# Kernel tuning notes

Measured on AMD Instinct MI355X. Metric: run time of the kernel, lower is better.

Reference implementation:

```python
import jax, jax.numpy as jnp
import numpy as np

EMB_DIM = 128
MID = 192  # ceil(1.5 * emb_dim)
VOCAB = 3000
KCLS = 5
B = 16
S = 128
EPS = 1e-5


def _linear_init(k, fin, fout):
    k1, k2 = jax.random.split(k)
    bound = 1.0 / np.sqrt(fin)
    W = jax.random.uniform(k1, (fin, fout), minval=-bound, maxval=bound, dtype=jnp.float32)
    b = jax.random.uniform(k2, (fout,), minval=-bound, maxval=bound, dtype=jnp.float32)
    return W, b


def setup_inputs() -> dict:
    key = jax.random.key(0)
    ks = jax.random.split(key, 7)
    emb = jax.random.normal(ks[0], (VOCAB, EMB_DIM), dtype=jnp.float32)
    W1, b1 = _linear_init(ks[1], 2 * EMB_DIM, MID)   # encoder layer 1
    W2, b2 = _linear_init(ks[2], MID, EMB_DIM)       # encoder layer 2
    W3, b3 = _linear_init(ks[3], EMB_DIM, MID)       # decoder layer 1
    W4, b4 = _linear_init(ks[4], MID, 2 * EMB_DIM)   # decoder layer 2
    Wk, bk = _linear_init(ks[5], EMB_DIM, KCLS)      # soft head
    inputs = jax.random.randint(ks[6], (B, S), 0, VOCAB, dtype=jnp.int64)
    return dict(inputs=inputs, emb=emb, W1=W1, b1=b1, W2=W2, b2=b2,
                W3=W3, b3=b3, W4=W4, b4=b4, Wk=Wk, bk=bk)


def _forward(inputs, emb, W1, b1, W2, b2, W3, b3, W4, b4, Wk, bk):
    X = emb[inputs]                      # (B,S,m)
    Bs, Sl, m = X.shape
    bidx = jnp.arange(Bs)
    karr = jnp.arange(Sl)
    jarr = jnp.arange(Sl - 1)

    def step(carry, t):
        nodes, counts, acc = carry       # (B,S,m), (B,S), (B,)
        L = Sl - t                       # current active list length
        right, left = nodes[:, 1:], nodes[:, :-1]          # pair j = (node[j+1], node[j])
        y = (jnp.concatenate([right, left], -1) @ W1 + b1) @ W2 + b2   # (B,S-1,m)
        xx = (y @ W3 + b3) @ W4 + b4                                    # (B,S-1,2m)
        # torch cross_entropy with float-vector target: -sum(target * log_softmax(input))
        ls1 = -(right * jax.nn.log_softmax(xx[..., :m], -1)).sum(-1)
        ls2 = -(left * jax.nn.log_softmax(xx[..., m:], -1)).sum(-1)
        n1, n2 = counts[:, 1:], counts[:, :-1]
        loss = ((n1 + EPS) * ls1 + (n2 + EPS) * ls2) / (n1 + n2 + EPS)
        valid = jarr < (L - 1)                                          # only first L-1 pairs active
        idx = jnp.argmin(jnp.where(valid[None, :], loss, jnp.inf), axis=1)  # (B,)
        acc = acc + jnp.take_along_axis(loss, idx[:, None], 1)[:, 0]
        father_x = jnp.take_along_axis(y, idx[:, None, None], 1)[:, 0]  # (B,m)
        # faithful bug: lc = nodelist[idx-1] (python wrap to L-1 when idx==0), rc = nodelist[idx]
        lc_idx = jnp.where(idx == 0, L - 1, idx - 1)
        father_cnt = (jnp.take_along_axis(counts, idx[:, None], 1)[:, 0]
                      + jnp.take_along_axis(counts, lc_idx[:, None], 1)[:, 0])
        pos = jnp.maximum(idx - 1, 0)
        # new list: drop lc and rc, father lands at pos; gather map reproduces list insert/remove
        src = jnp.where((idx[:, None] == 0) | (karr[None, :] < idx[:, None] - 1),
                        karr[None, :], karr[None, :] + 1)
        src = jnp.minimum(src, Sl - 1)
        nodes = jnp.take_along_axis(nodes, src[:, :, None], 1).at[bidx, pos].set(father_x)
        counts = jnp.take_along_axis(counts, src, 1).at[bidx, pos].set(father_cnt)
        return (nodes, counts, acc), None

    init = (X, jnp.ones((Bs, Sl), X.dtype), jnp.zeros((Bs,), X.dtype))
    (nodes, counts, acc), _ = jax.lax.scan(step, init, jnp.arange(Sl - 1))
    pred = jnp.argmax(nodes[:, 0] @ Wk + bk, axis=-1)   # argmax softmax == argmax logits
    return pred, acc.sum() / Bs


def reference(inputs, emb, W1, b1, W2, b2, W3, b3, W4, b4, Wk, bk):
    return _forward(inputs, emb, W1, b1, W2, b2, W3, b3, W4, b4, Wk, bk)
```

## Files before the change

kernel.cpp:

```cpp
#include <hip/hip_runtime.h>
#include <math.h>

#define EMB 128
#define MID 192
#define SEQ 128
#define BATCH 16
#define NPAIR 127
#define KCLS 5
#define EPSF 1e-5f

#define OFF_WYT   0
#define OFF_BY    32768
#define OFF_WXXT  32896
#define OFF_BXX   65664
#define OFF_NODES 65920
#define OFF_YC    328064
#define OFF_L0    588160

__global__ void k_comp(const float* __restrict__ W1, const float* __restrict__ b1,
                       const float* __restrict__ W2, const float* __restrict__ b2,
                       const float* __restrict__ W3, const float* __restrict__ b3,
                       const float* __restrict__ W4, const float* __restrict__ b4,
                       float* __restrict__ ws) {
    int tid = blockIdx.x * blockDim.x + threadIdx.x;
    if (tid < 32768) {
        int k = tid >> 7, o = tid & 127;
        float a = 0.f;
        for (int j = 0; j < MID; ++j) a += W1[k*MID+j] * W2[j*EMB+o];
        int q = k >> 6, jj = k & 63;
        ws[OFF_WYT + (size_t)(q*128 + o)*64 + jj] = a;
    } else if (tid < 65536) {
        int t = tid - 32768;
        int k = t >> 8, c = t & 255;
        float a = 0.f;
        for (int j = 0; j < MID; ++j) a += W3[k*MID+j] * W4[j*256+c];
        int hh = k >> 6, jj = k & 63;
        ws[OFF_WXXT + (size_t)(hh*256 + c)*64 + jj] = a;
    } else if (tid < 65536 + 128) {
        int o = tid - 65536;
        float a = b2[o];
        for (int j = 0; j < MID; ++j) a += b1[j] * W2[j*EMB+o];
        ws[OFF_BY + o] = a;
    } else if (tid < 65536 + 128 + 256) {
        int o = tid - 65536 - 128;
        float a = b4[o];
        for (int j = 0; j < MID; ++j) a += b3[j] * W4[j*256+o];
        ws[OFF_BXX + o] = a;
    }
}

__global__ void k_nodes(const int* __restrict__ inp, const float* __restrict__ emb,
                        float* __restrict__ ws) {
    int tid = blockIdx.x * blockDim.x + threadIdx.x;
    if (tid >= BATCH*SEQ*EMB) return;
    int d = tid & 127;
    int bs = tid >> 7;
    int tok = inp[bs];
    ws[OFF_NODES + tid] = emb[tok*EMB + d];
}

__global__ void __launch_bounds__(512, 2) k_init(float* __restrict__ ws) {
    __shared__ float s_x[2][2*EMB];
    __shared__ float s_red[4][2][EMB];
    __shared__ float s_redx[2][2][256];
    __shared__ float s_y[2][EMB];
    __shared__ float s_by[EMB];
    __shared__ float s_bxx[2*EMB];
    __shared__ float s_ls[2][2];
    int tid = threadIdx.x;
    int b = blockIdx.x >> 4, g = blockIdx.x & 15;
    float4 wy4[16], wxx4[16];
    {
        const float4* gw = (const float4*)(ws + OFF_WYT) + (size_t)tid*16;
        #pragma unroll
        for (int i = 0; i < 16; ++i) wy4[i] = gw[i];
        const float4* gx = (const float4*)(ws + OFF_WXXT) + (size_t)tid*16;
        #pragma unroll
        for (int i = 0; i < 16; ++i) wxx4[i] = gx[i];
    }
    if (tid < EMB) s_by[tid] = ws[OFF_BY + tid];
    if (tid < 2*EMB) s_bxx[tid] = ws[OFF_BXX + tid];
    const float* nodes = ws + OFF_NODES + (size_t)b*SEQ*EMB;
    float* yc = ws + OFF_YC + (size_t)b*NPAIR*EMB;
    int q4 = tid >> 7, o = tid & 127;
    int hh = tid >> 8, c = tid & 255;
    int p_s = tid >> 8, kk = tid & 255;
    __syncthreads();
    for (int it = 0; it < 4; ++it) {
        int base = g*8 + it*2;
        {
            int j = base + p_s;
            int jj = j < NPAIR ? j : NPAIR - 1;
            s_x[p_s][kk] = nodes[(jj + (kk < 128 ? 1 : 0))*EMB + (kk & 127)];
        }
        __syncthreads();
        {
            const float4* sx4 = (const float4*)s_x;
            float a0 = 0.f, a1 = 0.f;
            #pragma unroll
            for (int i = 0; i < 16; ++i) {
                float4 w = wy4[i];
                float4 x0 = sx4[q4*16 + i];
                float4 x1 = sx4[64 + q4*16 + i];
                a0 += x0.x*w.x + x0.y*w.y + x0.z*w.z + x0.w*w.w;
                a1 += x1.x*w.x + x1.y*w.y + x1.z*w.z + x1.w*w.w;
            }
            s_red[q4][0][o] = a0;
            s_red[q4][1][o] = a1;
        }
        __syncthreads();
        if (tid < 256) {
            int p = tid >> 7, oo = tid & 127;
            float yv = s_red[0][p][oo] + s_red[1][p][oo] + s_red[2][p][oo] + s_red[3][p][oo] + s_by[oo];
            s_y[p][oo] = yv;
            int j2 = base + p;
            if (j2 < NPAIR) yc[(size_t)j2*EMB + oo] = yv;
        }
        __syncthreads();
        {
            const float4* sy4 = (const float4*)s_y;
            float c0 = 0.f, c1 = 0.f;
            #pragma unroll
            for (int i = 0; i < 16; ++i) {
                float4 w = wxx4[i];
                float4 y0 = sy4[hh*16 + i];
                float4 y1 = sy4[32 + hh*16 + i];
                c0 += y0.x*w.x + y0.y*w.y + y0.z*w.z + y0.w*w.w;
                c1 += y1.x*w.x + y1.y*w.y + y1.z*w.z + y1.w*w.w;
            }
            s_redx[hh][0][c] = c0;
            s_redx[hh][1][c] = c1;
        }
        __syncthreads();
        if (tid < 256) {
            int w = tid >> 6, lane = tid & 63;
            int p2 = w >> 1, h2 = w & 1;
            int cA = h2*128 + lane, cB = cA + 64;
            float v0 = s_redx[0][p2][cA] + s_redx[1][p2][cA] + s_bxx[cA];
            float v1 = s_redx[0][p2][cB] + s_redx[1][p2][cB] + s_bxx[cB];
            float m = fmaxf(v0, v1);
            for (int s = 32; s; s >>= 1) m = fmaxf(m, __shfl_xor(m, s, 64));
            float se = expf(v0 - m) + expf(v1 - m);
            for (int s = 32; s; s >>= 1) se += __shfl_xor(se, s, 64);
            float lse = m + logf(se);
            float o0 = s_x[p2][cA], o1 = s_x[p2][cB];
            float term = o0*(v0 - lse) + o1*(v1 - lse);
            for (int s = 32; s; s >>= 1) term += __shfl_xor(term, s, 64);
            if (lane == 0) s_ls[p2][h2] = -term;
        }
        __syncthreads();
        if (tid < 2) {
            int j2 = base + tid;
            if (j2 < NPAIR) {
                float l = ((1.f+EPSF)*s_ls[tid][0] + (1.f+EPSF)*s_ls[tid][1]) / (2.f + EPSF);
                ws[OFF_L0 + b*NPAIR + j2] = l;
            }
        }
        __syncthreads();
    }
}

__global__ void __launch_bounds__(512, 2) k_seq(float* __restrict__ ws,
                      const float* __restrict__ Wk, const float* __restrict__ bkv,
                      float* __restrict__ out) {
    __shared__ float s_nodes[SEQ*EMB];
    __shared__ float s_yc[NPAIR*EMB];
    __shared__ float s_red[4][2][EMB];
    __shared__ float s_redx[2][2][256];
    __shared__ float s_y[2][EMB];
    __shared__ float s_by[EMB];
    __shared__ float s_bxx[2*EMB];
    __shared__ float s_ls[2][2];
    __shared__ float s_loss[NPAIR];
    __shared__ float s_cnt[SEQ];
    __shared__ int   s_nslot[SEQ];
    __shared__ int   s_yslot[NPAIR];
    __shared__ int   s_q[2];
    __shared__ float s_wv[2];
    __shared__ int   s_wi[2];
    __shared__ float s_log[KCLS];

    int tid = threadIdx.x;
    int b = blockIdx.x;
    float4 wy4[16], wxx4[16];
    {
        const float4* gw = (const float4*)(ws + OFF_WYT) + (size_t)tid*16;
        #pragma unroll
        for (int i = 0; i < 16; ++i) wy4[i] = gw[i];
        const float4* gx = (const float4*)(ws + OFF_WXXT) + (size_t)tid*16;
        #pragma unroll
        for (int i = 0; i < 16; ++i) wxx4[i] = gx[i];
    }
    {
        const float4* gn = (const float4*)(ws + OFF_NODES + (size_t)b*SEQ*EMB);
        float4* sn = (float4*)s_nodes;
        for (int i = tid; i < SEQ*EMB/4; i += 512) sn[i] = gn[i];
        const float4* gy = (const float4*)(ws + OFF_YC + (size_t)b*NPAIR*EMB);
        float4* sy = (float4*)s_yc;
        for (int i = tid; i < NPAIR*EMB/4; i += 512) sy[i] = gy[i];
    }
    if (tid < EMB) s_by[tid] = ws[OFF_BY + tid];
    if (tid < 2*EMB) s_bxx[tid] = ws[OFF_BXX + tid];
    if (tid < NPAIR) { s_loss[tid] = ws[OFF_L0 + b*NPAIR + tid]; s_yslot[tid] = tid; }
    if (tid < SEQ)   { s_cnt[tid] = 1.f; s_nslot[tid] = tid; }
    float acc = 0.f;
    int q4 = tid >> 7, o = tid & 127;
    int hh = tid >> 8, c = tid & 255;
    __syncthreads();

    #pragma unroll 1
    for (int t = 0; t < NPAIR; ++t) {
        int L = SEQ - t;
        if (t > 0) {
            {
                int r = (q4 < 2) ? 1 : 0;
                int half = q4 & 1;
                int slot0 = s_nslot[s_q[0] + r];
                int slot1 = s_nslot[s_q[1] + r];
                const float4* n4 = (const float4*)s_nodes;
                int base0 = slot0*32 + half*16;
                int base1 = slot1*32 + half*16;
                float a0 = 0.f, a1 = 0.f;
                #pragma unroll
                for (int i = 0; i < 16; ++i) {
                    float4 w = wy4[i];
                    float4 x0 = n4[base0 + i];
                    float4 x1 = n4[base1 + i];
                    a0 += x0.x*w.x + x0.y*w.y + x0.z*w.z + x0.w*w.w;
                    a1 += x1.x*w.x + x1.y*w.y + x1.z*w.z + x1.w*w.w;
                }
                s_red[q4][0][o] = a0;
                s_red[q4][1][o] = a1;
            }
            __syncthreads();
            if (tid < 256) {
                int p = tid >> 7, oo = tid & 127;
                float yv = s_red[0][p][oo] + s_red[1][p][oo] + s_red[2][p][oo] + s_red[3][p][oo] + s_by[oo];
                s_y[p][oo] = yv;
                s_yc[(size_t)s_yslot[s_q[p]]*EMB + oo] = yv;
            }
            __syncthreads();
            {
                const float4* sy4 = (const float4*)s_y;
                float c0 = 0.f, c1 = 0.f;
                #pragma unroll
                for (int i = 0; i < 16; ++i) {
                    float4 w = wxx4[i];
                    float4 y0 = sy4[hh*16 + i];
                    float4 y1 = sy4[32 + hh*16 + i];
                    c0 += y0.x*w.x + y0.y*w.y + y0.z*w.z + y0.w*w.w;
                    c1 += y1.x*w.x + y1.y*w.y + y1.z*w.z + y1.w*w.w;
                }
                s_redx[hh][0][c] = c0;
                s_redx[hh][1][c] = c1;
            }
            __syncthreads();
            if (tid < 256) {
                int w = tid >> 6, lane = tid & 63;
                int p2 = w >> 1, h2 = w & 1;
                int cA = h2*128 + lane, cB = cA + 64;
                float v0 = s_redx[0][p2][cA] + s_redx[1][p2][cA] + s_bxx[cA];
                float v1 = s_redx[0][p2][cB] + s_redx[1][p2][cB] + s_bxx[cB];
                float m = fmaxf(v0, v1);
                for (int s = 32; s; s >>= 1) m = fmaxf(m, __shfl_xor(m, s, 64));
                float se = expf(v0 - m) + expf(v1 - m);
                for (int s = 32; s; s >>= 1) se += __shfl_xor(se, s, 64);
                float lse = m + logf(se);
                int slot = s_nslot[s_q[p2] + (h2 == 0 ? 1 : 0)];
                float o0 = s_nodes[slot*EMB + lane];
                float o1 = s_nodes[slot*EMB + 64 + lane];
                float term = o0*(v0 - lse) + o1*(v1 - lse);
                for (int s = 32; s; s >>= 1) term += __shfl_xor(term, s, 64);
                if (lane == 0) s_ls[p2][h2] = -term;
            }
            __syncthreads();
        }
        if (tid < 128) {
            float v = INFINITY;
            if (tid < L-1) {
                v = s_loss[tid];
                if (t > 0 && (tid == s_q[0] || tid == s_q[1])) {
                    int which = (tid == s_q[0]) ? 0 : 1;
                    float n1 = s_cnt[tid+1], n2 = s_cnt[tid];
                    v = ((n1+EPSF)*s_ls[which][0] + (n2+EPSF)*s_ls[which][1]) / (n1+n2+EPSF);
                    s_loss[tid] = v;
                }
            }
            int ii = tid;
            for (int s = 32; s; s >>= 1) {
                float ov = __shfl_xor(v, s, 64);
                int   oi = __shfl_xor(ii, s, 64);
                if (ov < v || (ov == v && oi < ii)) { v = ov; ii = oi; }
            }
            if ((tid & 63) == 0) { s_wv[tid>>6] = v; s_wi[tid>>6] = ii; }
        }
        __syncthreads();
        float bv0 = s_wv[0], bv1 = s_wv[1];
        int idx = (bv1 < bv0) ? s_wi[1] : s_wi[0];
        if (tid == 0) acc += fminf(bv0, bv1);
        int pos = idx > 0 ? idx - 1 : 0;
        int slotF = s_nslot[pos];
        int ysI   = s_yslot[idx];
        float fcnt = s_cnt[idx] + s_cnt[idx == 0 ? L-1 : idx-1];
        bool doShift = (idx > 0);
        bool shL = doShift && tid >= pos+1 && tid <= L-3;
        bool shC = doShift && tid >= pos+1 && tid <= L-2;
        float nl = 0.f, nc = 0.f; int nn = 0, ny = 0;
        if (shL) { nl = s_loss[tid+1]; ny = s_yslot[tid+1]; }
        if (shC) { nc = s_cnt[tid+1];  nn = s_nslot[tid+1]; }
        float fx = (tid < EMB) ? s_yc[(size_t)ysI*EMB + tid] : 0.f;
        __syncthreads();
        if (tid < EMB) s_nodes[slotF*EMB + tid] = fx;
        if (shL) { s_loss[tid] = nl; s_yslot[tid] = ny; }
        if (shC) { s_cnt[tid]  = nc; s_nslot[tid] = nn; }
        if (tid == 0) {
            s_cnt[pos] = fcnt;
            s_q[0] = (pos >= 1) ? pos - 1 : pos;
            s_q[1] = pos;
        }
        __syncthreads();
    }
    if (tid < KCLS) {
        int slot0 = s_nslot[0];
        float a = bkv[tid];
        for (int k = 0; k < EMB; ++k) a += s_nodes[slot0*EMB + k] * Wk[k*KCLS + tid];
        s_log[tid] = a;
    }
    __syncthreads();
    if (tid == 0) {
        int best = 0;
        for (int cc = 1; cc < KCLS; ++cc) if (s_log[cc] > s_log[best]) best = cc;
        out[b] = (float)best;
        atomicAdd(&out[BATCH], acc * (1.f/16.f));
    }
}

extern "C" void kernel_launch(void* const* d_in, const int* in_sizes, int n_in,
                              void* d_out, int out_size, void* d_ws, size_t ws_size,
                              hipStream_t stream) {
    const int*   inp = (const int*)d_in[0];
    const float* emb = (const float*)d_in[1];
    const float* W1  = (const float*)d_in[2];
    const float* b1  = (const float*)d_in[3];
    const float* W2  = (const float*)d_in[4];
    const float* b2  = (const float*)d_in[5];
    const float* W3  = (const float*)d_in[6];
    const float* b3  = (const float*)d_in[7];
    const float* W4  = (const float*)d_in[8];
    const float* b4  = (const float*)d_in[9];
    const float* Wk  = (const float*)d_in[10];
    const float* bk  = (const float*)d_in[11];
    float* out = (float*)d_out;
    float* ws  = (float*)d_ws;

    hipMemsetAsync(d_out, 0, (size_t)out_size * sizeof(float), stream);

    k_comp<<<(65920 + 255) / 256, 256, 0, stream>>>(W1, b1, W2, b2, W3, b3, W4, b4, ws);
    k_nodes<<<(BATCH*SEQ*EMB + 255) / 256, 256, 0, stream>>>(inp, emb, ws);
    k_init<<<BATCH * 16, 512, 0, stream>>>(ws);
    k_seq<<<BATCH, 512, 0, stream>>>(ws, Wk, bk, out);
}
```

Before: 566.0 us.

## Move decoder weight to LDS and keep node/pair state in global memory

```diff
diff --git a/kernel.cpp b/kernel.cpp
--- a/kernel.cpp
+++ b/kernel.cpp
@@ -11,7 +11,7 @@
 
 #define OFF_WYT   0
 #define OFF_BY    32768
-#define OFF_WXXT  32896
+#define OFF_WXX   32896
 #define OFF_BXX   65664
 #define OFF_NODES 65920
 #define OFF_YC    328064
@@ -34,8 +34,7 @@
         int k = t >> 8, c = t & 255;
         float a = 0.f;
         for (int j = 0; j < MID; ++j) a += W3[k*MID+j] * W4[j*256+c];
-        int hh = k >> 6, jj = k & 63;
-        ws[OFF_WXXT + (size_t)(hh*256 + c)*64 + jj] = a;
+        ws[OFF_WXX + (size_t)k*256 + c] = a;
     } else if (tid < 65536 + 128) {
         int o = tid - 65536;
         float a = b2[o];
@@ -60,6 +59,7 @@
 }
 
 __global__ void __launch_bounds__(512, 2) k_init(float* __restrict__ ws) {
+    __shared__ float s_wxx[128*256];
     __shared__ float s_x[2][2*EMB];
     __shared__ float s_red[4][2][EMB];
     __shared__ float s_redx[2][2][256];
@@ -69,14 +69,14 @@
     __shared__ float s_ls[2][2];
     int tid = threadIdx.x;
     int b = blockIdx.x >> 4, g = blockIdx.x & 15;
-    float4 wy4[16], wxx4[16];
+    float4 wy4[16];
     {
         const float4* gw = (const float4*)(ws + OFF_WYT) + (size_t)tid*16;
         #pragma unroll
         for (int i = 0; i < 16; ++i) wy4[i] = gw[i];
-        const float4* gx = (const float4*)(ws + OFF_WXXT) + (size_t)tid*16;
-        #pragma unroll
-        for (int i = 0; i < 16; ++i) wxx4[i] = gx[i];
+        const float4* gx = (const float4*)(ws + OFF_WXX);
+        float4* sw = (float4*)s_wxx;
+        for (int i = tid; i < 8192; i += 512) sw[i] = gx[i];
     }
     if (tid < EMB) s_by[tid] = ws[OFF_BY + tid];
     if (tid < 2*EMB) s_bxx[tid] = ws[OFF_BXX + tid];
@@ -118,15 +118,15 @@
         }
         __syncthreads();
         {
-            const float4* sy4 = (const float4*)s_y;
+            const float* wp = s_wxx + (hh << 6)*256 + c;
+            const float* yp0 = &s_y[0][hh << 6];
+            const float* yp1 = &s_y[1][hh << 6];
             float c0 = 0.f, c1 = 0.f;
             #pragma unroll
-            for (int i = 0; i < 16; ++i) {
-                float4 w = wxx4[i];
-                float4 y0 = sy4[hh*16 + i];
-                float4 y1 = sy4[32 + hh*16 + i];
-                c0 += y0.x*w.x + y0.y*w.y + y0.z*w.z + y0.w*w.w;
-                c1 += y1.x*w.x + y1.y*w.y + y1.z*w.z + y1.w*w.w;
+            for (int j = 0; j < 64; ++j) {
+                float w = wp[j*256];
+                c0 += yp0[j] * w;
+                c1 += yp1[j] * w;
             }
             s_redx[hh][0][c] = c0;
             s_redx[hh][1][c] = c1;
@@ -163,8 +163,8 @@
 __global__ void __launch_bounds__(512, 2) k_seq(float* __restrict__ ws,
                       const float* __restrict__ Wk, const float* __restrict__ bkv,
                       float* __restrict__ out) {
-    __shared__ float s_nodes[SEQ*EMB];
-    __shared__ float s_yc[NPAIR*EMB];
+    __shared__ float s_wxx[128*256];
+    __shared__ float s_x[2][2*EMB];
     __shared__ float s_red[4][2][EMB];
     __shared__ float s_redx[2][2][256];
     __shared__ float s_y[2][EMB];
@@ -182,23 +182,17 @@
 
     int tid = threadIdx.x;
     int b = blockIdx.x;
-    float4 wy4[16], wxx4[16];
+    float4 wy4[16];
     {
         const float4* gw = (const float4*)(ws + OFF_WYT) + (size_t)tid*16;
         #pragma unroll
         for (int i = 0; i < 16; ++i) wy4[i] = gw[i];
-        const float4* gx = (const float4*)(ws + OFF_WXXT) + (size_t)tid*16;
-        #pragma unroll
-        for (int i = 0; i < 16; ++i) wxx4[i] = gx[i];
-    }
-    {
-        const float4* gn = (const float4*)(ws + OFF_NODES + (size_t)b*SEQ*EMB);
-        float4* sn = (float4*)s_nodes;
-        for (int i = tid; i < SEQ*EMB/4; i += 512) sn[i] = gn[i];
-        const float4* gy = (const float4*)(ws + OFF_YC + (size_t)b*NPAIR*EMB);
-        float4* sy = (float4*)s_yc;
-        for (int i = tid; i < NPAIR*EMB/4; i += 512) sy[i] = gy[i];
-    }
+        const float4* gx = (const float4*)(ws + OFF_WXX);
+        float4* sw = (float4*)s_wxx;
+        for (int i = tid; i < 8192; i += 512) sw[i] = gx[i];
+    }
+    float* nodes = ws + OFF_NODES + (size_t)b*SEQ*EMB;
+    float* yc    = ws + OFF_YC    + (size_t)b*NPAIR*EMB;
     if (tid < EMB) s_by[tid] = ws[OFF_BY + tid];
     if (tid < 2*EMB) s_bxx[tid] = ws[OFF_BXX + tid];
     if (tid < NPAIR) { s_loss[tid] = ws[OFF_L0 + b*NPAIR + tid]; s_yslot[tid] = tid; }
@@ -206,6 +200,7 @@
     float acc = 0.f;
     int q4 = tid >> 7, o = tid & 127;
     int hh = tid >> 8, c = tid & 255;
+    int p_s = tid >> 8, kk = tid & 255;
     __syncthreads();
 
     #pragma unroll 1
@@ -213,19 +208,18 @@
         int L = SEQ - t;
         if (t > 0) {
             {
-                int r = (q4 < 2) ? 1 : 0;
-                int half = q4 & 1;
-                int slot0 = s_nslot[s_q[0] + r];
-                int slot1 = s_nslot[s_q[1] + r];
-                const float4* n4 = (const float4*)s_nodes;
-                int base0 = slot0*32 + half*16;
-                int base1 = slot1*32 + half*16;
+                int q = s_q[p_s];
+                s_x[p_s][kk] = nodes[s_nslot[q + (kk < 128 ? 1 : 0)]*EMB + (kk & 127)];
+            }
+            __syncthreads();
+            {
+                const float4* sx4 = (const float4*)s_x;
                 float a0 = 0.f, a1 = 0.f;
                 #pragma unroll
                 for (int i = 0; i < 16; ++i) {
                     float4 w = wy4[i];
-                    float4 x0 = n4[base0 + i];
-                    float4 x1 = n4[base1 + i];
+                    float4 x0 = sx4[q4*16 + i];
+                    float4 x1 = sx4[64 + q4*16 + i];
                     a0 += x0.x*w.x + x0.y*w.y + x0.z*w.z + x0.w*w.w;
                     a1 += x1.x*w.x + x1.y*w.y + x1.z*w.z + x1.w*w.w;
                 }
@@ -237,19 +231,19 @@
                 int p = tid >> 7, oo = tid & 127;
                 float yv = s_red[0][p][oo] + s_red[1][p][oo] + s_red[2][p][oo] + s_red[3][p][oo] + s_by[oo];
                 s_y[p][oo] = yv;
-                s_yc[(size_t)s_yslot[s_q[p]]*EMB + oo] = yv;
+                yc[(size_t)s_yslot[s_q[p]]*EMB + oo] = yv;
             }
             __syncthreads();
             {
-                const float4* sy4 = (const float4*)s_y;
+                const float* wp = s_wxx + (hh << 6)*256 + c;
+                const float* yp0 = &s_y[0][hh << 6];
+                const float* yp1 = &s_y[1][hh << 6];
                 float c0 = 0.f, c1 = 0.f;
                 #pragma unroll
-                for (int i = 0; i < 16; ++i) {
-                    float4 w = wxx4[i];
-                    float4 y0 = sy4[hh*16 + i];
-                    float4 y1 = sy4[32 + hh*16 + i];
-                    c0 += y0.x*w.x + y0.y*w.y + y0.z*w.z + y0.w*w.w;
-                    c1 += y1.x*w.x + y1.y*w.y + y1.z*w.z + y1.w*w.w;
+                for (int j = 0; j < 64; ++j) {
+                    float w = wp[j*256];
+                    c0 += yp0[j] * w;
+                    c1 += yp1[j] * w;
                 }
                 s_redx[hh][0][c] = c0;
                 s_redx[hh][1][c] = c1;
@@ -266,9 +260,7 @@
                 float se = expf(v0 - m) + expf(v1 - m);
                 for (int s = 32; s; s >>= 1) se += __shfl_xor(se, s, 64);
                 float lse = m + logf(se);
-                int slot = s_nslot[s_q[p2] + (h2 == 0 ? 1 : 0)];
-                float o0 = s_nodes[slot*EMB + lane];
-                float o1 = s_nodes[slot*EMB + 64 + lane];
+                float o0 = s_x[p2][cA], o1 = s_x[p2][cB];
                 float term = o0*(v0 - lse) + o1*(v1 - lse);
                 for (int s = 32; s; s >>= 1) term += __shfl_xor(term, s, 64);
                 if (lane == 0) s_ls[p2][h2] = -term;
@@ -308,9 +300,9 @@
         float nl = 0.f, nc = 0.f; int nn = 0, ny = 0;
         if (shL) { nl = s_loss[tid+1]; ny = s_yslot[tid+1]; }
         if (shC) { nc = s_cnt[tid+1];  nn = s_nslot[tid+1]; }
-        float fx = (tid < EMB) ? s_yc[(size_t)ysI*EMB + tid] : 0.f;
-        __syncthreads();
-        if (tid < EMB) s_nodes[slotF*EMB + tid] = fx;
+        float fx = (tid < EMB) ? yc[(size_t)ysI*EMB + tid] : 0.f;
+        __syncthreads();
+        if (tid < EMB) nodes[slotF*EMB + tid] = fx;
         if (shL) { s_loss[tid] = nl; s_yslot[tid] = ny; }
         if (shC) { s_cnt[tid]  = nc; s_nslot[tid] = nn; }
         if (tid == 0) {
@@ -323,7 +315,7 @@
     if (tid < KCLS) {
         int slot0 = s_nslot[0];
         float a = bkv[tid];
-        for (int k = 0; k < EMB; ++k) a += s_nodes[slot0*EMB + k] * Wk[k*KCLS + tid];
+        for (int k = 0; k < EMB; ++k) a += nodes[slot0*EMB + k] * Wk[k*KCLS + tid];
         s_log[tid] = a;
     }
     __syncthreads();
```

Result: slower. 636.2 us (+12.4%).

## Use 1024-thread blocks and double-buffer list state to drop a barrier

Applied to the files above, without the earlier changes.

```diff
diff --git a/kernel.cpp b/kernel.cpp
--- a/kernel.cpp
+++ b/kernel.cpp
@@ -11,7 +11,7 @@
 
 #define OFF_WYT   0
 #define OFF_BY    32768
-#define OFF_WXXT  32896
+#define OFF_WXX   32896
 #define OFF_BXX   65664
 #define OFF_NODES 65920
 #define OFF_YC    328064
@@ -27,15 +27,15 @@
         int k = tid >> 7, o = tid & 127;
         float a = 0.f;
         for (int j = 0; j < MID; ++j) a += W1[k*MID+j] * W2[j*EMB+o];
-        int q = k >> 6, jj = k & 63;
-        ws[OFF_WYT + (size_t)(q*128 + o)*64 + jj] = a;
+        int q8 = k >> 5, jj = k & 31;
+        ws[OFF_WYT + ((q8*128 + o) << 5) + jj] = a;
     } else if (tid < 65536) {
         int t = tid - 32768;
         int k = t >> 8, c = t & 255;
         float a = 0.f;
         for (int j = 0; j < MID; ++j) a += W3[k*MID+j] * W4[j*256+c];
-        int hh = k >> 6, jj = k & 63;
-        ws[OFF_WXXT + (size_t)(hh*256 + c)*64 + jj] = a;
+        int h4 = k >> 5, jj = k & 31;
+        ws[OFF_WXX + ((h4*256 + c) << 5) + jj] = a;
     } else if (tid < 65536 + 128) {
         int o = tid - 65536;
         float a = b2[o];
@@ -59,36 +59,36 @@
     ws[OFF_NODES + tid] = emb[tok*EMB + d];
 }
 
-__global__ void __launch_bounds__(512, 2) k_init(float* __restrict__ ws) {
+__global__ void __launch_bounds__(1024) k_init(float* __restrict__ ws) {
     __shared__ float s_x[2][2*EMB];
-    __shared__ float s_red[4][2][EMB];
-    __shared__ float s_redx[2][2][256];
+    __shared__ float s_red[8][2][EMB];
+    __shared__ float s_redx[4][2][256];
     __shared__ float s_y[2][EMB];
     __shared__ float s_by[EMB];
     __shared__ float s_bxx[2*EMB];
     __shared__ float s_ls[2][2];
     int tid = threadIdx.x;
     int b = blockIdx.x >> 4, g = blockIdx.x & 15;
-    float4 wy4[16], wxx4[16];
+    float4 wy8[8], wxx8[8];
     {
-        const float4* gw = (const float4*)(ws + OFF_WYT) + (size_t)tid*16;
+        const float4* gw = (const float4*)(ws + OFF_WYT) + (size_t)tid*8;
         #pragma unroll
-        for (int i = 0; i < 16; ++i) wy4[i] = gw[i];
-        const float4* gx = (const float4*)(ws + OFF_WXXT) + (size_t)tid*16;
+        for (int i = 0; i < 8; ++i) wy8[i] = gw[i];
+        const float4* gx = (const float4*)(ws + OFF_WXX) + (size_t)tid*8;
         #pragma unroll
-        for (int i = 0; i < 16; ++i) wxx4[i] = gx[i];
+        for (int i = 0; i < 8; ++i) wxx8[i] = gx[i];
     }
     if (tid < EMB) s_by[tid] = ws[OFF_BY + tid];
     if (tid < 2*EMB) s_bxx[tid] = ws[OFF_BXX + tid];
     const float* nodes = ws + OFF_NODES + (size_t)b*SEQ*EMB;
     float* yc = ws + OFF_YC + (size_t)b*NPAIR*EMB;
-    int q4 = tid >> 7, o = tid & 127;
-    int hh = tid >> 8, c = tid & 255;
-    int p_s = tid >> 8, kk = tid & 255;
+    int q8 = tid >> 7, o = tid & 127;
+    int h4 = tid >> 8, c = tid & 255;
     __syncthreads();
     for (int it = 0; it < 4; ++it) {
         int base = g*8 + it*2;
-        {
+        if (tid < 512) {
+            int p_s = tid >> 8, kk = tid & 255;
             int j = base + p_s;
             int jj = j < NPAIR ? j : NPAIR - 1;
             s_x[p_s][kk] = nodes[(jj + (kk < 128 ? 1 : 0))*EMB + (kk & 127)];
@@ -98,20 +98,22 @@
             const float4* sx4 = (const float4*)s_x;
             float a0 = 0.f, a1 = 0.f;
             #pragma unroll
-            for (int i = 0; i < 16; ++i) {
-                float4 w = wy4[i];
-                float4 x0 = sx4[q4*16 + i];
-                float4 x1 = sx4[64 + q4*16 + i];
+            for (int i = 0; i < 8; ++i) {
+                float4 w = wy8[i];
+                float4 x0 = sx4[q8*8 + i];
+                float4 x1 = sx4[64 + q8*8 + i];
                 a0 += x0.x*w.x + x0.y*w.y + x0.z*w.z + x0.w*w.w;
                 a1 += x1.x*w.x + x1.y*w.y + x1.z*w.z + x1.w*w.w;
             }
-            s_red[q4][0][o] = a0;
-            s_red[q4][1][o] = a1;
+            s_red[q8][0][o] = a0;
+            s_red[q8][1][o] = a1;
         }
         __syncthreads();
         if (tid < 256) {
             int p = tid >> 7, oo = tid & 127;
-            float yv = s_red[0][p][oo] + s_red[1][p][oo] + s_red[2][p][oo] + s_red[3][p][oo] + s_by[oo];
+            float yv = s_by[oo];
+            #pragma unroll
+            for (int q = 0; q < 8; ++q) yv += s_red[q][p][oo];
             s_y[p][oo] = yv;
             int j2 = base + p;
             if (j2 < NPAIR) yc[(size_t)j2*EMB + oo] = yv;
@@ -121,23 +123,23 @@
             const float4* sy4 = (const float4*)s_y;
             float c0 = 0.f, c1 = 0.f;
             #pragma unroll
-            for (int i = 0; i < 16; ++i) {
-                float4 w = wxx4[i];
-                float4 y0 = sy4[hh*16 + i];
-                float4 y1 = sy4[32 + hh*16 + i];
+            for (int i = 0; i < 8; ++i) {
+                float4 w = wxx8[i];
+                float4 y0 = sy4[h4*8 + i];
+                float4 y1 = sy4[32 + h4*8 + i];
                 c0 += y0.x*w.x + y0.y*w.y + y0.z*w.z + y0.w*w.w;
                 c1 += y1.x*w.x + y1.y*w.y + y1.z*w.z + y1.w*w.w;
             }
-            s_redx[hh][0][c] = c0;
-            s_redx[hh][1][c] = c1;
+            s_redx[h4][0][c] = c0;
+            s_redx[h4][1][c] = c1;
         }
         __syncthreads();
         if (tid < 256) {
             int w = tid >> 6, lane = tid & 63;
             int p2 = w >> 1, h2 = w & 1;
             int cA = h2*128 + lane, cB = cA + 64;
-            float v0 = s_redx[0][p2][cA] + s_redx[1][p2][cA] + s_bxx[cA];
-            float v1 = s_redx[0][p2][cB] + s_redx[1][p2][cB] + s_bxx[cB];
+            float v0 = s_redx[0][p2][cA] + s_redx[1][p2][cA] + s_redx[2][p2][cA] + s_redx[3][p2][cA] + s_bxx[cA];
+            float v1 = s_redx[0][p2][cB] + s_redx[1][p2][cB] + s_redx[2][p2][cB] + s_redx[3][p2][cB] + s_bxx[cB];
             float m = fmaxf(v0, v1);
             for (int s = 32; s; s >>= 1) m = fmaxf(m, __shfl_xor(m, s, 64));
             float se = expf(v0 - m) + expf(v1 - m);
@@ -160,21 +162,21 @@
     }
 }
 
-__global__ void __launch_bounds__(512, 2) k_seq(float* __restrict__ ws,
+__global__ void __launch_bounds__(1024) k_seq(float* __restrict__ ws,
                       const float* __restrict__ Wk, const float* __restrict__ bkv,
                       float* __restrict__ out) {
     __shared__ float s_nodes[SEQ*EMB];
     __shared__ float s_yc[NPAIR*EMB];
-    __shared__ float s_red[4][2][EMB];
-    __shared__ float s_redx[2][2][256];
+    __shared__ float s_red[8][2][EMB];
+    __shared__ float s_redx[4][2][256];
     __shared__ float s_y[2][EMB];
     __shared__ float s_by[EMB];
     __shared__ float s_bxx[2*EMB];
     __shared__ float s_ls[2][2];
-    __shared__ float s_loss[NPAIR];
-    __shared__ float s_cnt[SEQ];
-    __shared__ int   s_nslot[SEQ];
-    __shared__ int   s_yslot[NPAIR];
+    __shared__ float s_loss[2][NPAIR];
+    __shared__ float s_cnt[2][SEQ];
+    __shared__ int   s_nslot[2][SEQ];
+    __shared__ int   s_yslot[2][NPAIR];
     __shared__ int   s_q[2];
     __shared__ float s_wv[2];
     __shared__ int   s_wi[2];
@@ -182,91 +184,94 @@
 
     int tid = threadIdx.x;
     int b = blockIdx.x;
-    float4 wy4[16], wxx4[16];
+    float4 wy8[8], wxx8[8];
     {
-        const float4* gw = (const float4*)(ws + OFF_WYT) + (size_t)tid*16;
+        const float4* gw = (const float4*)(ws + OFF_WYT) + (size_t)tid*8;
         #pragma unroll
-        for (int i = 0; i < 16; ++i) wy4[i] = gw[i];
-        const float4* gx = (const float4*)(ws + OFF_WXXT) + (size_t)tid*16;
+        for (int i = 0; i < 8; ++i) wy8[i] = gw[i];
+        const float4* gx = (const float4*)(ws + OFF_WXX) + (size_t)tid*8;
         #pragma unroll
-        for (int i = 0; i < 16; ++i) wxx4[i] = gx[i];
+        for (int i = 0; i < 8; ++i) wxx8[i] = gx[i];
     }
     {
         const float4* gn = (const float4*)(ws + OFF_NODES + (size_t)b*SEQ*EMB);
         float4* sn = (float4*)s_nodes;
-        for (int i = tid; i < SEQ*EMB/4; i += 512) sn[i] = gn[i];
+        for (int i = tid; i < SEQ*EMB/4; i += 1024) sn[i] = gn[i];
         const float4* gy = (const float4*)(ws + OFF_YC + (size_t)b*NPAIR*EMB);
         float4* sy = (float4*)s_yc;
-        for (int i = tid; i < NPAIR*EMB/4; i += 512) sy[i] = gy[i];
+        for (int i = tid; i < NPAIR*EMB/4; i += 1024) sy[i] = gy[i];
     }
     if (tid < EMB) s_by[tid] = ws[OFF_BY + tid];
     if (tid < 2*EMB) s_bxx[tid] = ws[OFF_BXX + tid];
-    if (tid < NPAIR) { s_loss[tid] = ws[OFF_L0 + b*NPAIR + tid]; s_yslot[tid] = tid; }
-    if (tid < SEQ)   { s_cnt[tid] = 1.f; s_nslot[tid] = tid; }
+    if (tid < NPAIR) { s_loss[0][tid] = ws[OFF_L0 + b*NPAIR + tid]; s_yslot[0][tid] = tid; }
+    if (tid < SEQ)   { s_cnt[0][tid] = 1.f; s_nslot[0][tid] = tid; }
     float acc = 0.f;
-    int q4 = tid >> 7, o = tid & 127;
-    int hh = tid >> 8, c = tid & 255;
+    int q8 = tid >> 7, o = tid & 127;
+    int h4 = tid >> 8, c = tid & 255;
     __syncthreads();
 
     #pragma unroll 1
     for (int t = 0; t < NPAIR; ++t) {
         int L = SEQ - t;
+        int cur = t & 1, nxt = cur ^ 1;
         if (t > 0) {
             {
-                int r = (q4 < 2) ? 1 : 0;
-                int half = q4 & 1;
-                int slot0 = s_nslot[s_q[0] + r];
-                int slot1 = s_nslot[s_q[1] + r];
+                int r = (q8 < 4) ? 1 : 0;
+                int slot0 = s_nslot[cur][s_q[0] + r];
+                int slot1 = s_nslot[cur][s_q[1] + r];
                 const float4* n4 = (const float4*)s_nodes;
-                int base0 = slot0*32 + half*16;
-                int base1 = slot1*32 + half*16;
+                int sub = (q8 & 3) * 8;
+                int base0 = slot0*32 + sub;
+                int base1 = slot1*32 + sub;
                 float a0 = 0.f, a1 = 0.f;
                 #pragma unroll
-                for (int i = 0; i < 16; ++i) {
-                    float4 w = wy4[i];
+                for (int i = 0; i < 8; ++i) {
+                    float4 w = wy8[i];
                     float4 x0 = n4[base0 + i];
                     float4 x1 = n4[base1 + i];
                     a0 += x0.x*w.x + x0.y*w.y + x0.z*w.z + x0.w*w.w;
                     a1 += x1.x*w.x + x1.y*w.y + x1.z*w.z + x1.w*w.w;
                 }
-                s_red[q4][0][o] = a0;
-                s_red[q4][1][o] = a1;
+                s_red[q8][0][o] = a0;
+                s_red[q8][1][o] = a1;
             }
             __syncthreads();
             if (tid < 256) {
                 int p = tid >> 7, oo = tid & 127;
-                float yv = s_red[0][p][oo] + s_red[1][p][oo] + s_red[2][p][oo] + s_red[3][p][oo] + s_by[oo];
+                float yv = s_by[oo];
+                #pragma unroll
+                for (int q = 0; q < 8; ++q) yv += s_red[q][p][oo];
                 s_y[p][oo] = yv;
-                s_yc[(size_t)s_yslot[s_q[p]]*EMB + oo] = yv;
+                s_yc[(size_t)s_yslot[cur][s_q[p]]*EMB + oo] = yv;
             }
             __syncthreads();
             {
                 const float4* sy4 = (const float4*)s_y;
                 float c0 = 0.f, c1 = 0.f;
                 #pragma unroll
-                for (int i = 0; i < 16; ++i) {
-                    float4 w = wxx4[i];
-                    float4 y0 = sy4[hh*16 + i];
-                    float4 y1 = sy4[32 + hh*16 + i];
+                for (int i = 0; i < 8; ++i) {
+                    float4 w = wxx8[i];
+                    float4 y0 = sy4[h4*8 + i];
+                    float4 y1 = sy4[32 + h4*8 + i];
                     c0 += y0.x*w.x + y0.y*w.y + y0.z*w.z + y0.w*w.w;
                     c1 += y1.x*w.x + y1.y*w.y + y1.z*w.z + y1.w*w.w;
                 }
-                s_redx[hh][0][c] = c0;
-                s_redx[hh][1][c] = c1;
+                s_redx[h4][0][c] = c0;
+                s_redx[h4][1][c] = c1;
             }
             __syncthreads();
             if (tid < 256) {
                 int w = tid >> 6, lane = tid & 63;
                 int p2 = w >> 1, h2 = w & 1;
                 int cA = h2*128 + lane, cB = cA + 64;
-                float v0 = s_redx[0][p2][cA] + s_redx[1][p2][cA] + s_bxx[cA];
-                float v1 = s_redx[0][p2][cB] + s_redx[1][p2][cB] + s_bxx[cB];
+                float v0 = s_redx[0][p2][cA] + s_redx[1][p2][cA] + s_redx[2][p2][cA] + s_redx[3][p2][cA] + s_bxx[cA];
+                float v1 = s_redx[0][p2][cB] + s_redx[1][p2][cB] + s_redx[2][p2][cB] + s_redx[3][p2][cB] + s_bxx[cB];
                 float m = fmaxf(v0, v1);
                 for (int s = 32; s; s >>= 1) m = fmaxf(m, __shfl_xor(m, s, 64));
                 float se = expf(v0 - m) + expf(v1 - m);
                 for (int s = 32; s; s >>= 1) se += __shfl_xor(se, s, 64);
                 float lse = m + logf(se);
-                int slot = s_nslot[s_q[p2] + (h2 == 0 ? 1 : 0)];
+                int slot = s_nslot[cur][s_q[p2] + (h2 == 0 ? 1 : 0)];
                 float o0 = s_nodes[slot*EMB + lane];
                 float o1 = s_nodes[slot*EMB + 64 + lane];
                 float term = o0*(v0 - lse) + o1*(v1 - lse);
@@ -278,12 +283,12 @@
         if (tid < 128) {
             float v = INFINITY;
             if (tid < L-1) {
-                v = s_loss[tid];
+                v = s_loss[cur][tid];
                 if (t > 0 && (tid == s_q[0] || tid == s_q[1])) {
                     int which = (tid == s_q[0]) ? 0 : 1;
-                    float n1 = s_cnt[tid+1], n2 = s_cnt[tid];
+                    float n1 = s_cnt[cur][tid+1], n2 = s_cnt[cur][tid];
                     v = ((n1+EPSF)*s_ls[which][0] + (n2+EPSF)*s_ls[which][1]) / (n1+n2+EPSF);
-                    s_loss[tid] = v;
+                    s_loss[cur][tid] = v;
                 }
             }
             int ii = tid;
@@ -295,33 +300,41 @@
             if ((tid & 63) == 0) { s_wv[tid>>6] = v; s_wi[tid>>6] = ii; }
         }
         __syncthreads();
-        float bv0 = s_wv[0], bv1 = s_wv[1];
-        int idx = (bv1 < bv0) ? s_wi[1] : s_wi[0];
-        if (tid == 0) acc += fminf(bv0, bv1);
-        int pos = idx > 0 ? idx - 1 : 0;
-        int slotF = s_nslot[pos];
-        int ysI   = s_yslot[idx];
-        float fcnt = s_cnt[idx] + s_cnt[idx == 0 ? L-1 : idx-1];
-        bool doShift = (idx > 0);
-        bool shL = doShift && tid >= pos+1 && tid <= L-3;
-        bool shC = doShift && tid >= pos+1 && tid <= L-2;
-        float nl = 0.f, nc = 0.f; int nn = 0, ny = 0;
-        if (shL) { nl = s_loss[tid+1]; ny = s_yslot[tid+1]; }
-        if (shC) { nc = s_cnt[tid+1];  nn = s_nslot[tid+1]; }
-        float fx = (tid < EMB) ? s_yc[(size_t)ysI*EMB + tid] : 0.f;
-        __syncthreads();
-        if (tid < EMB) s_nodes[slotF*EMB + tid] = fx;
-        if (shL) { s_loss[tid] = nl; s_yslot[tid] = ny; }
-        if (shC) { s_cnt[tid]  = nc; s_nslot[tid] = nn; }
-        if (tid == 0) {
-            s_cnt[pos] = fcnt;
-            s_q[0] = (pos >= 1) ? pos - 1 : pos;
-            s_q[1] = pos;
+        {
+            float bv0 = s_wv[0], bv1 = s_wv[1];
+            int idx = (bv1 < bv0) ? s_wi[1] : s_wi[0];
+            if (tid == 0) acc += fminf(bv0, bv1);
+            int pos = idx > 0 ? idx - 1 : 0;
+            bool doShift = (idx > 0);
+            if (tid < 128) {
+                int sC = (doShift && tid >= pos+1 && tid <= L-2) ? 1 : 0;
+                float nc = s_cnt[cur][tid + sC];
+                int   nn = s_nslot[cur][tid + sC];
+                if (tid == pos) {
+                    float fcnt = s_cnt[cur][idx] + s_cnt[cur][idx == 0 ? L-1 : idx-1];
+                    nc = fcnt;
+                }
+                s_cnt[nxt][tid] = nc;
+                s_nslot[nxt][tid] = nn;
+                if (tid < NPAIR) {
+                    int sL = (doShift && tid >= pos+1 && tid <= L-3) ? 1 : 0;
+                    s_loss[nxt][tid]  = s_loss[cur][tid + sL];
+                    s_yslot[nxt][tid] = s_yslot[cur][tid + sL];
+                }
+            } else if (tid < 256) {
+                int d = tid - 128;
+                int slotF = s_nslot[cur][pos];
+                int ysI   = s_yslot[cur][idx];
+                s_nodes[slotF*EMB + d] = s_yc[(size_t)ysI*EMB + d];
+            } else if (tid == 256) {
+                s_q[0] = (pos >= 1) ? pos - 1 : pos;
+                s_q[1] = pos;
+            }
         }
         __syncthreads();
     }
     if (tid < KCLS) {
-        int slot0 = s_nslot[0];
+        int slot0 = s_nslot[1][0];
         float a = bkv[tid];
         for (int k = 0; k < EMB; ++k) a += s_nodes[slot0*EMB + k] * Wk[k*KCLS + tid];
         s_log[tid] = a;
@@ -357,6 +370,6 @@
 
     k_comp<<<(65920 + 255) / 256, 256, 0, stream>>>(W1, b1, W2, b2, W3, b3, W4, b4, ws);
     k_nodes<<<(BATCH*SEQ*EMB + 255) / 256, 256, 0, stream>>>(inp, emb, ws);
-    k_init<<<BATCH * 16, 512, 0, stream>>>(ws);
-    k_seq<<<BATCH, 512, 0, stream>>>(ws, Wk, bk, out);
-}
+    k_init<<<BATCH * 16, 1024, 0, stream>>>(ws);
+    k_seq<<<BATCH, 1024, 0, stream>>>(ws, Wk, bk, out);
+}
```

Result: no change. 560.4 us (-1.0%).
